# Kernel tuning notes

Hardware: AMD Instinct MI355X
Metric: run time of the kernel (lower is better)

The kernel has to match this reference:

```python
import jax, jax.numpy as jnp
import numpy as np

NH = 8        # num_heads
KS = 64       # key_size
C_IN = 256
C_OUT = 3 * NH * KS   # 1536
GROUPS = 3 * NH       # 24
EPS = 1e-5
H = W = 64


def setup_inputs() -> dict:
    key = jax.random.key(0)
    k1, k2 = jax.random.split(key)
    x = jax.random.normal(k1, (1, C_IN, H, W), dtype=jnp.float32)
    conv_w = jax.random.normal(k2, (C_OUT, C_IN, 1, 1), dtype=jnp.float32) * 0.05
    gn_w = jnp.ones((C_OUT,), dtype=jnp.float32)
    gn_b = jnp.zeros((C_OUT,), dtype=jnp.float32)
    return {"x": x, "conv_w": conv_w, "gn_w": gn_w, "gn_b": gn_b}


def reference(x, conv_w, gn_w, gn_b):
    B, _, h, w = x.shape
    # 1x1 conv (normalize=True -> no bias): per-pixel GEMM over channels
    attn = jnp.einsum('bchw,oc->bohw', x, conv_w[:, :, 0, 0])  # [B, 1536, H, W]
    # GroupNorm: 24 groups of KS channels, normalized over (KS, H, W)
    g = attn.reshape(B, GROUPS, -1)
    mean = g.mean(axis=-1, keepdims=True)
    var = g.var(axis=-1, keepdims=True)
    g = (g - mean) * jax.lax.rsqrt(var + EPS)
    attn = g.reshape(B, C_OUT, h, w) * gn_w[None, :, None, None] + gn_b[None, :, None, None]
    # split into key, query, value (in that order, per chunk(3, dim=2))
    attn = attn.reshape(B, NH, 3 * KS, h * w)
    key_, query, value = jnp.split(attn, 3, axis=2)   # each [B, NH, KS, HW]
    # saliency = q^T @ k / sqrt(KS) -> [B, NH, HW, HW]
    saliency = jnp.einsum('bnkq,bnkl->bnql', query, key_) / jnp.sqrt(jnp.float32(KS))
    mask = jax.nn.softmax(saliency, axis=-1)
    # out = v @ mask^T -> [B, NH, KS, HW]
    out = jnp.einsum('bnkl,bnql->bnkq', value, mask)
    return out.reshape(B, NH * KS, h, w)
```

## Files before the change

### kernel.cpp

```cpp
#include <hip/hip_runtime.h>

typedef __bf16 bf16;
typedef __bf16 bf16x8 __attribute__((ext_vector_type(8)));
typedef __bf16 bf16x4 __attribute__((ext_vector_type(4)));
typedef float f32x4 __attribute__((ext_vector_type(4)));
typedef float f32x16 __attribute__((ext_vector_type(16)));


#define QF 0.18033688011112042f
#define EXPF(x) __builtin_amdgcn_exp2f(x)

union U4 { bf16x4 v; unsigned u[2]; };
union U8 { bf16x8 v; unsigned u[4]; };

__global__ void k_misc(const float* __restrict__ x, const float* __restrict__ w,
                       bf16* __restrict__ xT, bf16* __restrict__ wb, float* __restrict__ cs) {
    int b = blockIdx.x;
    if (b < 256) {
        __shared__ float ld[64][65];
        int cb = (b & 3) * 64;
        int pb = (b >> 2) * 64;
        int tp = (threadIdx.x & 15) * 4;
        int tc = threadIdx.x >> 4;
#pragma unroll
        for (int pass = 0; pass < 4; pass++) {
            int c = tc + pass * 16;
            float4 f = *(const float4*)(x + (cb + c) * 4096 + pb + tp);
            ld[tp][c] = f.x; ld[tp + 1][c] = f.y; ld[tp + 2][c] = f.z; ld[tp + 3][c] = f.w;
        }
        __syncthreads();
        int px = threadIdx.x >> 3;
        int co = (threadIdx.x & 7) * 8;
#pragma unroll
        for (int pass = 0; pass < 2; pass++) {
            int p2 = px + pass * 32;
            bf16x8 o;
#pragma unroll
            for (int j = 0; j < 8; j++) o[j] = (bf16)ld[p2][co + j];
            *(bf16x8*)(xT + (pb + p2) * 256 + cb + co) = o;
        }
    } else if (b < 640) {
        int idx = ((b - 256) * 256 + threadIdx.x) * 4;
        float4 f = *(const float4*)(w + idx);
        bf16x4 o;
        o[0] = (bf16)f.x; o[1] = (bf16)f.y; o[2] = (bf16)f.z; o[3] = (bf16)f.w;
        *(bf16x4*)(wb + idx) = o;
    } else {
#pragma unroll
        for (int i = 0; i < 12; i++) cs[i * 256 + threadIdx.x] = 0.f;
    }
}

__global__ __launch_bounds__(256) void k_conv(const bf16* __restrict__ Wb,
                                              const bf16* __restrict__ xT,
                                              bf16* __restrict__ qkvT,
                                              float* __restrict__ cs) {
    __shared__ __attribute__((aligned(16))) bf16 xs[64 * 72];
    __shared__ __attribute__((aligned(16))) bf16 ws2[64 * 72];
    int wid = threadIdx.x >> 6, lane = threadIdx.x & 63;
    int quad = lane >> 4, l15 = lane & 15;
    int g  = blockIdx.x % 24;
    int pb = (blockIdx.x / 24) * 64;
    int h = g / 3, sec = g % 3;
    int ob = g * 64;

    int srow = threadIdx.x >> 2;
    int scol = (threadIdx.x & 3) * 16;

    f32x4 acc[4];
#pragma unroll
    for (int c = 0; c < 4; c++) acc[c] = (f32x4){0.f, 0.f, 0.f, 0.f};

    bf16x8 fx0 = *(const bf16x8*)(xT + (pb + srow) * 256 + scol);
    bf16x8 fx1 = *(const bf16x8*)(xT + (pb + srow) * 256 + scol + 8);
    bf16x8 fw0 = *(const bf16x8*)(Wb + (ob + srow) * 256 + scol);
    bf16x8 fw1 = *(const bf16x8*)(Wb + (ob + srow) * 256 + scol + 8);

    for (int c4 = 0; c4 < 4; c4++) {
        __syncthreads();
        *(bf16x8*)(xs  + srow * 72 + scol)     = fx0;
        *(bf16x8*)(xs  + srow * 72 + scol + 8) = fx1;
        *(bf16x8*)(ws2 + srow * 72 + scol)     = fw0;
        *(bf16x8*)(ws2 + srow * 72 + scol + 8) = fw1;
        __syncthreads();

        if (c4 < 3) {
            int co = (c4 + 1) * 64;
            fx0 = *(const bf16x8*)(xT + (pb + srow) * 256 + co + scol);
            fx1 = *(const bf16x8*)(xT + (pb + srow) * 256 + co + scol + 8);
            fw0 = *(const bf16x8*)(Wb + (ob + srow) * 256 + co + scol);
            fw1 = *(const bf16x8*)(Wb + (ob + srow) * 256 + co + scol + 8);
        }

#pragma unroll
        for (int k2 = 0; k2 < 2; k2++) {
            bf16x8 a = *(const bf16x8*)(ws2 + (wid * 16 + l15) * 72 + k2 * 32 + quad * 8);
#pragma unroll
            for (int c = 0; c < 4; c++) {
                bf16x8 b = *(const bf16x8*)(xs + (c * 16 + l15) * 72 + k2 * 32 + quad * 8);
                acc[c] = __builtin_amdgcn_mfma_f32_16x16x32_bf16(a, b, acc[c], 0, 0, 0);
            }
        }
    }

    int ch0 = wid * 16 + quad * 4;
#pragma unroll
    for (int r = 0; r < 4; r++) {
        float sp  = acc[0][r] + acc[1][r] + acc[2][r] + acc[3][r];
        float ssp = acc[0][r] * acc[0][r] + acc[1][r] * acc[1][r]
                  + acc[2][r] * acc[2][r] + acc[3][r] * acc[3][r];
#pragma unroll
        for (int m = 1; m < 16; m <<= 1) {
            sp  += __shfl_xor(sp,  m, 64);
            ssp += __shfl_xor(ssp, m, 64);
        }
        if (l15 == 0) {
            atomicAdd(cs + (ob + ch0 + r) * 2,     sp);
            atomicAdd(cs + (ob + ch0 + r) * 2 + 1, ssp);
        }
    }

    __syncthreads();
    bf16* tile = xs;
    if (sec == 2) {
#pragma unroll
        for (int c = 0; c < 4; c++)
#pragma unroll
            for (int r = 0; r < 4; r++)
                tile[(ch0 + r) * 72 + c * 16 + l15] = (bf16)acc[c][r];
    } else {
#pragma unroll
        for (int c = 0; c < 4; c++) {
            bf16x4 o;
#pragma unroll
            for (int r = 0; r < 4; r++) o[r] = (bf16)acc[c][r];
            *(bf16x4*)(&tile[(c * 16 + l15) * 72 + ch0]) = o;
        }
    }
    __syncthreads();
    bf16* base = qkvT + h * 786432;
    int t = threadIdx.x;
    if (sec == 2) {
        bf16* V = base + 524288;
#pragma unroll
        for (int it = 0; it < 2; it++) {
            int e = it * 256 + t; int ch = e >> 3; int pxo = (e & 7) * 8;
            *(bf16x8*)(V + ch * 4096 + pb + pxo) = *(const bf16x8*)(&tile[ch * 72 + pxo]);
        }
    } else {
        bf16* dst = base + (sec == 0 ? 262144 : 0);
#pragma unroll
        for (int it = 0; it < 2; it++) {
            int e = it * 256 + t; int px = e >> 3; int cho = (e & 7) * 8;
            *(bf16x8*)(dst + (pb + px) * 64 + cho) = *(const bf16x8*)(&tile[px * 72 + cho]);
        }
    }
}

#define PF_BLOCK(S, PFA, PFB)                                                   \
    {                                                                           \
        float p0 = EXPF(S[0]),  p1 = EXPF(S[1]),  p2 = EXPF(S[2]),  p3 = EXPF(S[3]);   \
        float p4 = EXPF(S[4]),  p5 = EXPF(S[5]),  p6 = EXPF(S[6]),  p7 = EXPF(S[7]);   \
        float p8 = EXPF(S[8]),  p9 = EXPF(S[9]),  p10 = EXPF(S[10]), p11 = EXPF(S[11]); \
        float p12 = EXPF(S[12]), p13 = EXPF(S[13]), p14 = EXPF(S[14]), p15 = EXPF(S[15]); \
        lacc += (((p0 + p1) + (p2 + p3)) + ((p4 + p5) + (p6 + p7)))             \
              + (((p8 + p9) + (p10 + p11)) + ((p12 + p13) + (p14 + p15)));      \
        U4 lo, hi;                                                              \
        lo.v[0] = (bf16)p0;  lo.v[1] = (bf16)p1;  lo.v[2] = (bf16)p2;  lo.v[3] = (bf16)p3;  \
        hi.v[0] = (bf16)p4;  hi.v[1] = (bf16)p5;  hi.v[2] = (bf16)p6;  hi.v[3] = (bf16)p7;  \
        unsigned a0 = lo.u[0], b0 = hi.u[0], a1 = lo.u[1], b1 = hi.u[1];        \
        asm("v_permlane32_swap_b32 %0, %1" : "+v"(a0), "+v"(b0));               \
        asm("v_permlane32_swap_b32 %0, %1" : "+v"(a1), "+v"(b1));               \
        U8 fA; fA.u[0] = a0; fA.u[1] = a1; fA.u[2] = b0; fA.u[3] = b1;          \
        PFA = fA.v;                                                             \
        U4 lo2, hi2;                                                            \
        lo2.v[0] = (bf16)p8;  lo2.v[1] = (bf16)p9;  lo2.v[2] = (bf16)p10; lo2.v[3] = (bf16)p11; \
        hi2.v[0] = (bf16)p12; hi2.v[1] = (bf16)p13; hi2.v[2] = (bf16)p14; hi2.v[3] = (bf16)p15; \
        unsigned a2 = lo2.u[0], b2 = hi2.u[0], a3 = lo2.u[1], b3 = hi2.u[1];    \
        asm("v_permlane32_swap_b32 %0, %1" : "+v"(a2), "+v"(b2));               \
        asm("v_permlane32_swap_b32 %0, %1" : "+v"(a3), "+v"(b3));               \
        U8 fB; fB.u[0] = a2; fB.u[1] = a3; fB.u[2] = b2; fB.u[3] = b3;          \
        PFB = fB.v;                                                             \
    }

__global__ __launch_bounds__(256, 4) void k_attn(const bf16* __restrict__ qkvT,
                                                 const float2* __restrict__ cs,
                                                 const float* __restrict__ gnw,
                                                 const float* __restrict__ gnb,
                                                 bf16* __restrict__ Opart,
                                                 float* __restrict__ Lsum) {
    int bid   = blockIdx.x;
    int h     = bid & 7;
    int qb    = (bid >> 3) & 31;
    int split = bid >> 8;
    int wid = threadIdx.x >> 6, lane = threadIdx.x & 63;
    int l31 = lane & 31, half = lane >> 5;
    const bf16* QT = qkvT + h * 786432;
    const bf16* KT = QT + 262144;
    const bf16* V  = QT + 524288;
    int qw = qb * 128 + wid * 32;

    __shared__ __attribute__((aligned(16))) bf16 Ks[2][64 * 72];
    __shared__ __attribute__((aligned(16))) bf16 Vs[2][64 * 72];

    int r0   = threadIdx.x >> 3;
    int koff = (threadIdx.x & 7) * 8;

    float2 vK = cs[(h * 3) * 64 + lane];
    float2 vQ = cs[(h * 3 + 1) * 64 + lane];
    float sK = vK.x, qK = vK.y, sQ = vQ.x, qQ = vQ.y;
#pragma unroll
    for (int m = 1; m < 64; m <<= 1) {
        sK += __shfl_xor(sK, m, 64); qK += __shfl_xor(qK, m, 64);
        sQ += __shfl_xor(sQ, m, 64); qQ += __shfl_xor(qQ, m, 64);
    }
    const float N = 262144.0f;
    float meanK = sK / N, invK = rsqrtf(qK / N - meanK * meanK + 1e-5f);
    float meanQ = sQ / N, invQ = rsqrtf(qQ / N - meanQ * meanQ + 1e-5f);

    bf16x8 bq[4];
#pragma unroll
    for (int ks = 0; ks < 4; ks++) {
        bf16x8 raw = *(const bf16x8*)(QT + (qw + l31) * 64 + ks * 16 + half * 8);
#pragma unroll
        for (int j = 0; j < 8; j++) {
            int c = ks * 16 + half * 8 + j;
            float gwq = gnw[h * 192 + 64 + c] * invQ;
            float qv  = (gwq * (float)raw[j] + (gnb[h * 192 + 64 + c] - meanQ * gwq)) * QF;
            float aKc = gnw[h * 192 + c] * invK;
            bq[ks][j] = (bf16)(aKc * qv);
        }
    }

    f32x16 oacc0 = (f32x16)(0.0f), oacc1 = (f32x16)(0.0f);
    float ls = 0.f;

    int t0 = split * 16, t1 = t0 + 16;

    bf16x8 kf0, kf1, vf0, vf1;
    {
        int lb0 = t0 * 64;
        kf0 = *(const bf16x8*)(KT + (lb0 + r0) * 64 + koff);
        kf1 = *(const bf16x8*)(KT + (lb0 + r0 + 32) * 64 + koff);
        vf0 = *(const bf16x8*)(V + r0 * 4096 + lb0 + koff);
        vf1 = *(const bf16x8*)(V + (r0 + 32) * 4096 + lb0 + koff);
    }

    for (int lt = t0; lt < t1; lt++) {
        bf16* ksb = Ks[lt & 1];
        bf16* vsb = Vs[lt & 1];

        *(bf16x8*)(ksb + r0 * 72 + koff)        = kf0;
        *(bf16x8*)(ksb + (r0 + 32) * 72 + koff) = kf1;
        *(bf16x8*)(vsb + r0 * 72 + koff)        = vf0;
        *(bf16x8*)(vsb + (r0 + 32) * 72 + koff) = vf1;
        __syncthreads();

        if (lt + 1 < t1) {
            int nb = (lt + 1) * 64;
            kf0 = *(const bf16x8*)(KT + (nb + r0) * 64 + koff);
            kf1 = *(const bf16x8*)(KT + (nb + r0 + 32) * 64 + koff);
            vf0 = *(const bf16x8*)(V + r0 * 4096 + nb + koff);
            vf1 = *(const bf16x8*)(V + (r0 + 32) * 4096 + nb + koff);
        }

        const bf16* ka = ksb + l31 * 72 + half * 8;
        const bf16* kb = ksb + (32 + l31) * 72 + half * 8;
        f32x16 s0 = (f32x16)(0.0f), s1 = (f32x16)(0.0f);
        __builtin_amdgcn_s_setprio(1);
#pragma unroll
        for (int ks = 0; ks < 4; ks++) {
            s0 = __builtin_amdgcn_mfma_f32_32x32x16_bf16(
                *(const bf16x8*)(ka + ks * 16), bq[ks], s0, 0, 0, 0);
            s1 = __builtin_amdgcn_mfma_f32_32x32x16_bf16(
                *(const bf16x8*)(kb + ks * 16), bq[ks], s1, 0, 0, 0);
        }
        __builtin_amdgcn_s_setprio(0);

        float lacc = ls;
        bf16x8 pf0, pf1, pf2, pf3;
        PF_BLOCK(s0, pf0, pf1);
        PF_BLOCK(s1, pf2, pf3);
        ls = lacc;

        const bf16* va = vsb + l31 * 72 + half * 8;
        const bf16* vb = vsb + (32 + l31) * 72 + half * 8;
        __builtin_amdgcn_s_setprio(1);
        oacc0 = __builtin_amdgcn_mfma_f32_32x32x16_bf16(*(const bf16x8*)(va +  0), pf0, oacc0, 0, 0, 0);
        oacc1 = __builtin_amdgcn_mfma_f32_32x32x16_bf16(*(const bf16x8*)(vb +  0), pf0, oacc1, 0, 0, 0);
        oacc0 = __builtin_amdgcn_mfma_f32_32x32x16_bf16(*(const bf16x8*)(va + 16), pf1, oacc0, 0, 0, 0);
        oacc1 = __builtin_amdgcn_mfma_f32_32x32x16_bf16(*(const bf16x8*)(vb + 16), pf1, oacc1, 0, 0, 0);
        oacc0 = __builtin_amdgcn_mfma_f32_32x32x16_bf16(*(const bf16x8*)(va + 32), pf2, oacc0, 0, 0, 0);
        oacc1 = __builtin_amdgcn_mfma_f32_32x32x16_bf16(*(const bf16x8*)(vb + 32), pf2, oacc1, 0, 0, 0);
        oacc0 = __builtin_amdgcn_mfma_f32_32x32x16_bf16(*(const bf16x8*)(va + 48), pf3, oacc0, 0, 0, 0);
        oacc1 = __builtin_amdgcn_mfma_f32_32x32x16_bf16(*(const bf16x8*)(vb + 48), pf3, oacc1, 0, 0, 0);
        __builtin_amdgcn_s_setprio(0);
    }

    ls += __shfl_xor(ls, 32, 64);
    if (half == 0)
        Lsum[split * 32768 + h * 4096 + qw + l31] = ls;

    bf16* Ob = Opart + split * 2097152;
#pragma unroll
    for (int r = 0; r < 16; r++) {
        int kd = (r & 3) + 8 * (r >> 2) + 4 * half;
        Ob[(h * 64 + kd) * 4096 + qw + l31]        = (bf16)oacc0[r];
        Ob[(h * 64 + 32 + kd) * 4096 + qw + l31]   = (bf16)oacc1[r];
    }
}

__global__ void k_final(const bf16* __restrict__ Opart, const float* __restrict__ Lsum,
                        const float2* __restrict__ cs, const float* __restrict__ gnw,
                        const float* __restrict__ gnb, float* __restrict__ out) {
    int gid = blockIdx.x * 256 + threadIdx.x;
    int row = gid >> 9;
    int c8  = (gid & 511) << 3;
    int h   = row >> 6;

    int g = h * 3 + 2;
    int c = threadIdx.x & 63;
    float2 v = cs[g * 64 + c];
    float s = v.x, ss = v.y;
#pragma unroll
    for (int m = 1; m < 64; m <<= 1) { s += __shfl_xor(s, m, 64); ss += __shfl_xor(ss, m, 64); }
    const float N = 262144.0f;
    float mean = s / N;
    float inv  = rsqrtf(ss / N - mean * mean + 1e-5f);
    int gi = h * 192 + 128 + (row & 63);
    float gw = gnw[gi];
    float va = inv * gw;
    float vb = gnb[gi] - mean * inv * gw;

    float o[8] = {0, 0, 0, 0, 0, 0, 0, 0};
    float l[8] = {0, 0, 0, 0, 0, 0, 0, 0};
#pragma unroll
    for (int sp = 0; sp < 4; sp++) {
        bf16x8 vv = *(const bf16x8*)(Opart + sp * 2097152 + row * 4096 + c8);
        const float* L = Lsum + sp * 32768 + h * 4096 + c8;
        float4 l0 = *(const float4*)L;
        float4 l1 = *(const float4*)(L + 4);
#pragma unroll
        for (int j = 0; j < 8; j++) o[j] += (float)vv[j];
        l[0] += l0.x; l[1] += l0.y; l[2] += l0.z; l[3] += l0.w;
        l[4] += l1.x; l[5] += l1.y; l[6] += l1.z; l[7] += l1.w;
    }
    float4 r0, r1;
    r0.x = va * o[0] / l[0] + vb; r0.y = va * o[1] / l[1] + vb;
    r0.z = va * o[2] / l[2] + vb; r0.w = va * o[3] / l[3] + vb;
    r1.x = va * o[4] / l[4] + vb; r1.y = va * o[5] / l[5] + vb;
    r1.z = va * o[6] / l[6] + vb; r1.w = va * o[7] / l[7] + vb;
    *(float4*)(out + row * 4096 + c8)     = r0;
    *(float4*)(out + row * 4096 + c8 + 4) = r1;
}

extern "C" void kernel_launch(void* const* d_in, const int* in_sizes, int n_in,
                              void* d_out, int out_size, void* d_ws, size_t ws_size,
                              hipStream_t stream) {
    const float* x      = (const float*)d_in[0];
    const float* conv_w = (const float*)d_in[1];
    const float* gn_w   = (const float*)d_in[2];
    const float* gn_b   = (const float*)d_in[3];
    float* out = (float*)d_out;
    char* ws = (char*)d_ws;

    bf16*   qkvT  = (bf16*) (ws);
    bf16*   Opart = (bf16*) (ws + 12582912);
    bf16*   Wb    = (bf16*) (ws + 12582912);
    bf16*   xT    = (bf16*) (ws + 13369344);
    float*  Lsum  = (float*)(ws + 29360128);
    float*  cs    = (float*)(ws + 29884416);

    hipLaunchKernelGGL(k_misc,  dim3(641),  dim3(256), 0, stream, x, conv_w, xT, Wb, cs);
    hipLaunchKernelGGL(k_conv,  dim3(1536), dim3(256), 0, stream, Wb, xT, qkvT, cs);
    hipLaunchKernelGGL(k_attn,  dim3(1024), dim3(256), 0, stream, qkvT, (const float2*)cs,
                       gn_w, gn_b, Opart, Lsum);
    hipLaunchKernelGGL(k_final, dim3(1024), dim3(256), 0, stream, Opart, Lsum, (const float2*)cs, gn_w, gn_b, out);
}
```

Before: 133.5 us.

## Software-pipeline QK and PV MFMAs across tiles and use three KV splits

Restructures the attention loop so the QK^T MFMAs for tile t are issued together with the PV MFMAs for tile t-1. This lets the softmax/exp work overlap with matrix-core work, and it adds an extra barrier per iteration to protect the double-buffered shared memory. The KV dimension is now split three ways instead of four, giving 768 blocks, and launch bounds drop to 3 blocks per CU to make room for the extra live registers. The tradeoffs are more register pressure, unequal split sizes (21/21/22 tiles), and the extra sync.

```diff
diff --git a/kernel.cpp b/kernel.cpp
--- a/kernel.cpp
+++ b/kernel.cpp
@@ -183,7 +183,49 @@
         PFB = fB.v;                                                             \
     }
 
-__global__ __launch_bounds__(256, 4) void k_attn(const bf16* __restrict__ qkvT,
+#define STAGE(BK, BV)                                                           \
+    *(bf16x8*)((BK) + r0 * 72 + koff)        = kf0;                             \
+    *(bf16x8*)((BK) + (r0 + 32) * 72 + koff) = kf1;                             \
+    *(bf16x8*)((BV) + r0 * 72 + koff)        = vf0;                             \
+    *(bf16x8*)((BV) + (r0 + 32) * 72 + koff) = vf1;
+
+#define PREFETCH(T)                                                             \
+    {   int nb = (T) * 64;                                                      \
+        kf0 = *(const bf16x8*)(KT + (nb + r0) * 64 + koff);                     \
+        kf1 = *(const bf16x8*)(KT + (nb + r0 + 32) * 64 + koff);                \
+        vf0 = *(const bf16x8*)(V + r0 * 4096 + nb + koff);                      \
+        vf1 = *(const bf16x8*)(V + (r0 + 32) * 4096 + nb + koff); }
+
+#define QK_TILE(KSB)                                                            \
+    {   const bf16* ka = (KSB) + l31 * 72 + half * 8;                           \
+        const bf16* kb = (KSB) + (32 + l31) * 72 + half * 8;                    \
+        s0 = (f32x16)(0.0f); s1 = (f32x16)(0.0f);                               \
+        __builtin_amdgcn_s_setprio(1);                                          \
+        s0 = __builtin_amdgcn_mfma_f32_32x32x16_bf16(*(const bf16x8*)(ka +  0), bq[0], s0, 0, 0, 0); \
+        s1 = __builtin_amdgcn_mfma_f32_32x32x16_bf16(*(const bf16x8*)(kb +  0), bq[0], s1, 0, 0, 0); \
+        s0 = __builtin_amdgcn_mfma_f32_32x32x16_bf16(*(const bf16x8*)(ka + 16), bq[1], s0, 0, 0, 0); \
+        s1 = __builtin_amdgcn_mfma_f32_32x32x16_bf16(*(const bf16x8*)(kb + 16), bq[1], s1, 0, 0, 0); \
+        s0 = __builtin_amdgcn_mfma_f32_32x32x16_bf16(*(const bf16x8*)(ka + 32), bq[2], s0, 0, 0, 0); \
+        s1 = __builtin_amdgcn_mfma_f32_32x32x16_bf16(*(const bf16x8*)(kb + 32), bq[2], s1, 0, 0, 0); \
+        s0 = __builtin_amdgcn_mfma_f32_32x32x16_bf16(*(const bf16x8*)(ka + 48), bq[3], s0, 0, 0, 0); \
+        s1 = __builtin_amdgcn_mfma_f32_32x32x16_bf16(*(const bf16x8*)(kb + 48), bq[3], s1, 0, 0, 0); \
+        __builtin_amdgcn_s_setprio(0); }
+
+#define PV_TILE(VSB)                                                            \
+    {   const bf16* va = (VSB) + l31 * 72 + half * 8;                           \
+        const bf16* vb = (VSB) + (32 + l31) * 72 + half * 8;                    \
+        __builtin_amdgcn_s_setprio(1);                                          \
+        oacc0 = __builtin_amdgcn_mfma_f32_32x32x16_bf16(*(const bf16x8*)(va +  0), pfp0, oacc0, 0, 0, 0); \
+        oacc1 = __builtin_amdgcn_mfma_f32_32x32x16_bf16(*(const bf16x8*)(vb +  0), pfp0, oacc1, 0, 0, 0); \
+        oacc0 = __builtin_amdgcn_mfma_f32_32x32x16_bf16(*(const bf16x8*)(va + 16), pfp1, oacc0, 0, 0, 0); \
+        oacc1 = __builtin_amdgcn_mfma_f32_32x32x16_bf16(*(const bf16x8*)(vb + 16), pfp1, oacc1, 0, 0, 0); \
+        oacc0 = __builtin_amdgcn_mfma_f32_32x32x16_bf16(*(const bf16x8*)(va + 32), pfp2, oacc0, 0, 0, 0); \
+        oacc1 = __builtin_amdgcn_mfma_f32_32x32x16_bf16(*(const bf16x8*)(vb + 32), pfp2, oacc1, 0, 0, 0); \
+        oacc0 = __builtin_amdgcn_mfma_f32_32x32x16_bf16(*(const bf16x8*)(va + 48), pfp3, oacc0, 0, 0, 0); \
+        oacc1 = __builtin_amdgcn_mfma_f32_32x32x16_bf16(*(const bf16x8*)(vb + 48), pfp3, oacc1, 0, 0, 0); \
+        __builtin_amdgcn_s_setprio(0); }
+
+__global__ __launch_bounds__(256, 3) void k_attn(const bf16* __restrict__ qkvT,
                                                  const float2* __restrict__ cs,
                                                  const float* __restrict__ gnw,
                                                  const float* __restrict__ gnb,
@@ -233,69 +275,41 @@
     }
 
     f32x16 oacc0 = (f32x16)(0.0f), oacc1 = (f32x16)(0.0f);
+    f32x16 s0, s1;
+    bf16x8 pfp0, pfp1, pfp2, pfp3;
     float ls = 0.f;
 
-    int t0 = split * 16, t1 = t0 + 16;
+    int t0 = (split * 64) / 3, t1 = ((split + 1) * 64) / 3;
 
     bf16x8 kf0, kf1, vf0, vf1;
+    PREFETCH(t0);
+
+    STAGE(Ks[t0 & 1], Vs[t0 & 1]);
+    __syncthreads();
+    if (t0 + 1 < t1) PREFETCH(t0 + 1);
+    QK_TILE(Ks[t0 & 1]);
     {
-        int lb0 = t0 * 64;
-        kf0 = *(const bf16x8*)(KT + (lb0 + r0) * 64 + koff);
-        kf1 = *(const bf16x8*)(KT + (lb0 + r0 + 32) * 64 + koff);
-        vf0 = *(const bf16x8*)(V + r0 * 4096 + lb0 + koff);
-        vf1 = *(const bf16x8*)(V + (r0 + 32) * 4096 + lb0 + koff);
-    }
-
-    for (int lt = t0; lt < t1; lt++) {
-        bf16* ksb = Ks[lt & 1];
-        bf16* vsb = Vs[lt & 1];
-
-        *(bf16x8*)(ksb + r0 * 72 + koff)        = kf0;
-        *(bf16x8*)(ksb + (r0 + 32) * 72 + koff) = kf1;
-        *(bf16x8*)(vsb + r0 * 72 + koff)        = vf0;
-        *(bf16x8*)(vsb + (r0 + 32) * 72 + koff) = vf1;
-        __syncthreads();
-
-        if (lt + 1 < t1) {
-            int nb = (lt + 1) * 64;
-            kf0 = *(const bf16x8*)(KT + (nb + r0) * 64 + koff);
-            kf1 = *(const bf16x8*)(KT + (nb + r0 + 32) * 64 + koff);
-            vf0 = *(const bf16x8*)(V + r0 * 4096 + nb + koff);
-            vf1 = *(const bf16x8*)(V + (r0 + 32) * 4096 + nb + koff);
-        }
-
-        const bf16* ka = ksb + l31 * 72 + half * 8;
-        const bf16* kb = ksb + (32 + l31) * 72 + half * 8;
-        f32x16 s0 = (f32x16)(0.0f), s1 = (f32x16)(0.0f);
-        __builtin_amdgcn_s_setprio(1);
-#pragma unroll
-        for (int ks = 0; ks < 4; ks++) {
-            s0 = __builtin_amdgcn_mfma_f32_32x32x16_bf16(
-                *(const bf16x8*)(ka + ks * 16), bq[ks], s0, 0, 0, 0);
-            s1 = __builtin_amdgcn_mfma_f32_32x32x16_bf16(
-                *(const bf16x8*)(kb + ks * 16), bq[ks], s1, 0, 0, 0);
-        }
-        __builtin_amdgcn_s_setprio(0);
-
         float lacc = ls;
-        bf16x8 pf0, pf1, pf2, pf3;
-        PF_BLOCK(s0, pf0, pf1);
-        PF_BLOCK(s1, pf2, pf3);
+        PF_BLOCK(s0, pfp0, pfp1);
+        PF_BLOCK(s1, pfp2, pfp3);
         ls = lacc;
-
-        const bf16* va = vsb + l31 * 72 + half * 8;
-        const bf16* vb = vsb + (32 + l31) * 72 + half * 8;
-        __builtin_amdgcn_s_setprio(1);
-        oacc0 = __builtin_amdgcn_mfma_f32_32x32x16_bf16(*(const bf16x8*)(va +  0), pf0, oacc0, 0, 0, 0);
-        oacc1 = __builtin_amdgcn_mfma_f32_32x32x16_bf16(*(const bf16x8*)(vb +  0), pf0, oacc1, 0, 0, 0);
-        oacc0 = __builtin_amdgcn_mfma_f32_32x32x16_bf16(*(const bf16x8*)(va + 16), pf1, oacc0, 0, 0, 0);
-        oacc1 = __builtin_amdgcn_mfma_f32_32x32x16_bf16(*(const bf16x8*)(vb + 16), pf1, oacc1, 0, 0, 0);
-        oacc0 = __builtin_amdgcn_mfma_f32_32x32x16_bf16(*(const bf16x8*)(va + 32), pf2, oacc0, 0, 0, 0);
-        oacc1 = __builtin_amdgcn_mfma_f32_32x32x16_bf16(*(const bf16x8*)(vb + 32), pf2, oacc1, 0, 0, 0);
-        oacc0 = __builtin_amdgcn_mfma_f32_32x32x16_bf16(*(const bf16x8*)(va + 48), pf3, oacc0, 0, 0, 0);
-        oacc1 = __builtin_amdgcn_mfma_f32_32x32x16_bf16(*(const bf16x8*)(vb + 48), pf3, oacc1, 0, 0, 0);
-        __builtin_amdgcn_s_setprio(0);
-    }
+    }
+
+    for (int lt = t0 + 1; lt < t1; lt++) {
+        __syncthreads();
+        STAGE(Ks[lt & 1], Vs[lt & 1]);
+        __syncthreads();
+        if (lt + 1 < t1) PREFETCH(lt + 1);
+        QK_TILE(Ks[lt & 1]);
+        PV_TILE(Vs[(lt - 1) & 1]);
+        {
+            float lacc = ls;
+            PF_BLOCK(s0, pfp0, pfp1);
+            PF_BLOCK(s1, pfp2, pfp3);
+            ls = lacc;
+        }
+    }
+    PV_TILE(Vs[(t1 - 1) & 1]);
 
     ls += __shfl_xor(ls, 32, 64);
     if (half == 0)
@@ -335,7 +349,7 @@
     float o[8] = {0, 0, 0, 0, 0, 0, 0, 0};
     float l[8] = {0, 0, 0, 0, 0, 0, 0, 0};
 #pragma unroll
-    for (int sp = 0; sp < 4; sp++) {
+    for (int sp = 0; sp < 3; sp++) {
         bf16x8 vv = *(const bf16x8*)(Opart + sp * 2097152 + row * 4096 + c8);
         const float* L = Lsum + sp * 32768 + h * 4096 + c8;
         float4 l0 = *(const float4*)L;
@@ -373,7 +387,7 @@
 
     hipLaunchKernelGGL(k_misc,  dim3(641),  dim3(256), 0, stream, x, conv_w, xT, Wb, cs);
     hipLaunchKernelGGL(k_conv,  dim3(1536), dim3(256), 0, stream, Wb, xT, qkvT, cs);
-    hipLaunchKernelGGL(k_attn,  dim3(1024), dim3(256), 0, stream, qkvT, (const float2*)cs,
+    hipLaunchKernelGGL(k_attn,  dim3(768),  dim3(256), 0, stream, qkvT, (const float2*)cs,
                        gn_w, gn_b, Opart, Lsum);
     hipLaunchKernelGGL(k_final, dim3(1024), dim3(256), 0, stream, Opart, Lsum, (const float2*)cs, gn_w, gn_b, out);
 }
```

After: 135.8 us. No clear change (+1.7%).
